# Performance work log

Hardware: AMD Instinct MI355X
Metric: run time of the kernel (lower is better)

The kernel has to match this reference:

```python
import jax, jax.numpy as jnp
import numpy as np

N, C, DK, DV = 8192, 128, 64, 64


def setup_inputs() -> dict:
    key = jax.random.key(0)
    ks = jax.random.split(key, 7)
    x = jax.random.normal(ks[0], (N, C), dtype=jnp.float32)
    # kaiming_normal for weights (std = sqrt(2/fan_in)), torch-default uniform bias
    std = float(np.sqrt(2.0 / C))
    bb = float(1.0 / np.sqrt(C))
    Wq = jax.random.normal(ks[1], (DK, C), dtype=jnp.float32) * std
    Wk = jax.random.normal(ks[2], (DK, C), dtype=jnp.float32) * std
    Wv = jax.random.normal(ks[3], (DV, C), dtype=jnp.float32) * std
    bq = jax.random.uniform(ks[4], (DK,), dtype=jnp.float32, minval=-bb, maxval=bb)
    bk = jax.random.uniform(ks[5], (DK,), dtype=jnp.float32, minval=-bb, maxval=bb)
    bv = jax.random.uniform(ks[6], (DV,), dtype=jnp.float32, minval=-bb, maxval=bb)
    return {"polyline_feature": x, "Wq": Wq, "bq": bq, "Wk": Wk, "bk": bk, "Wv": Wv, "bv": bv}


def reference(polyline_feature, Wq, bq, Wk, bk, Wv, bv):
    x = polyline_feature
    Q = jax.nn.relu(x @ Wq.T + bq)  # [N, DK]
    K = jax.nn.relu(x @ Wk.T + bk)  # [N, DK]
    V = jax.nn.relu(x @ Wv.T + bv)  # [N, DV]
    scores = (Q @ K.T) / jnp.sqrt(jnp.asarray(K.shape[1], Q.dtype))  # [N, N]
    attn = jax.nn.softmax(scores, axis=1)
    return attn @ V + Q  # residual on Q (non-standard)
```

## Files before the change

### kernel.cpp

```cpp
#include <hip/hip_runtime.h>


typedef __attribute__((ext_vector_type(8))) __bf16 bf16x8;
typedef __attribute__((ext_vector_type(4))) float f32x4;
typedef __attribute__((ext_vector_type(16))) float f32x16;

constexpr int N_ROWS = 8192;
constexpr int CDIM   = 128;
constexpr int DKV    = 64;
constexpr float SCALE_Q = 0.125f * 1.4426950408889634f;

__device__ __forceinline__ float fast_exp2(float x) {
    return __builtin_amdgcn_exp2f(x);
}

__device__ __forceinline__ unsigned short f2bf(float x) {
    union { float f; unsigned u; } v; v.f = x;
    unsigned r = v.u + 0x7fffu + ((v.u >> 16) & 1u);
    return (unsigned short)(r >> 16);
}

union Frag {
    unsigned u32[4];
    unsigned short u16[8];
    bf16x8 b;
    f32x4 f;
};

__global__ __launch_bounds__(128) void qkv_kernel(
    const float* __restrict__ x,
    const float* __restrict__ Wq, const float* __restrict__ bq,
    const float* __restrict__ Wk, const float* __restrict__ bk,
    const float* __restrict__ Wv, const float* __restrict__ bv,
    unsigned short* __restrict__ Qb, unsigned short* __restrict__ Kb,
    unsigned short* __restrict__ Vt, float* __restrict__ Qf)
{
    const int tid = threadIdx.x;
    const int w  = tid >> 6;
    const int l  = tid & 63;
    const int g  = l >> 4;
    const int lm = l & 15;
    const int n_base = blockIdx.x * 32 + w * 16;

    bf16x8 af[4];
    {
        const float* xrow = x + (size_t)(n_base + lm) * CDIM;
        #pragma unroll
        for (int s = 0; s < 4; ++s) {
            f32x4 lo = *(const f32x4*)(xrow + s * 32 + g * 8);
            f32x4 hi = *(const f32x4*)(xrow + s * 32 + g * 8 + 4);
            Frag fr;
            #pragma unroll
            for (int j = 0; j < 4; ++j) { fr.u16[j] = f2bf(lo[j]); fr.u16[4 + j] = f2bf(hi[j]); }
            af[s] = fr.b;
        }
    }

    const float* Ws[3] = {Wq, Wk, Wv};
    const float* Bs[3] = {bq, bk, bv};
    #pragma unroll
    for (int mat = 0; mat < 3; ++mat) {
        #pragma unroll
        for (int ct = 0; ct < 4; ++ct) {
            const int f = ct * 16 + lm;
            const float* wrow = Ws[mat] + (size_t)f * CDIM;
            f32x4 acc = {0.f, 0.f, 0.f, 0.f};
            #pragma unroll
            for (int s = 0; s < 4; ++s) {
                f32x4 lo = *(const f32x4*)(wrow + s * 32 + g * 8);
                f32x4 hi = *(const f32x4*)(wrow + s * 32 + g * 8 + 4);
                Frag fr;
                #pragma unroll
                for (int j = 0; j < 4; ++j) { fr.u16[j] = f2bf(lo[j]); fr.u16[4 + j] = f2bf(hi[j]); }
                acc = __builtin_amdgcn_mfma_f32_16x16x32_bf16(af[s], fr.b, acc, 0, 0, 0);
            }
            const float bias = Bs[mat][f];
            #pragma unroll
            for (int j = 0; j < 4; ++j) {
                const int n = n_base + g * 4 + j;
                const float v = fmaxf(acc[j] + bias, 0.f);
                if (mat == 0) {
                    Qf[(size_t)n * DKV + f] = v;
                    Qb[(size_t)n * DKV + f] = f2bf(v * SCALE_Q);
                } else if (mat == 1) {
                    Kb[(size_t)n * DKV + f] = f2bf(v);
                } else {
                    Vt[(size_t)f * N_ROWS + n] = f2bf(v);
                }
            }
        }
    }
}

__global__ __launch_bounds__(256, 4) void attn_kernel(
    const unsigned short* __restrict__ Qb, const unsigned short* __restrict__ Kb,
    const unsigned short* __restrict__ Vt,
    float* __restrict__ PartO, float* __restrict__ PartL,
    int kv_per_split)
{
    __shared__ __align__(16) unsigned short K_lds[2][64 * 64];
    __shared__ __align__(16) unsigned short V_lds[2][64 * 64];

    const int tid = threadIdx.x;
    const int w  = tid >> 6;
    const int l  = tid & 63;
    const int c  = l & 31;
    const int hB = l >> 5;
    const int qb = blockIdx.x;
    const int sp = blockIdx.y;
    const int q0 = qb * 128 + w * 32;
    const int kv0 = sp * kv_per_split;

    const int lrow = l >> 3;
    const int srcc = ((l & 7) ^ lrow) * 8;

#define ISSUE_LOADS(T, B) do { \
    const int kvt_ = kv0 + (T) * 64; \
    _Pragma("unroll") \
    for (int i = 0; i < 2; ++i) { \
        const int row_ = w * 16 + i * 8 + lrow; \
        __builtin_amdgcn_global_load_lds( \
            (const __attribute__((address_space(1))) unsigned int*)(Kb + (size_t)(kvt_ + row_) * DKV + srcc), \
            (__attribute__((address_space(3))) unsigned int*)&K_lds[B][(w * 16 + i * 8) * 64], 16, 0, 0); \
        __builtin_amdgcn_global_load_lds( \
            (const __attribute__((address_space(1))) unsigned int*)(Vt + (size_t)row_ * N_ROWS + kvt_ + srcc), \
            (__attribute__((address_space(3))) unsigned int*)&V_lds[B][(w * 16 + i * 8) * 64], 16, 0, 0); \
    } \
} while (0)

    bf16x8 qf0, qf1, qf2, qf3;
    {
        const unsigned short* qp = Qb + (size_t)(q0 + c) * DKV + hB * 8;
        qf0 = *(const bf16x8*)(qp);
        qf1 = *(const bf16x8*)(qp + 16);
        qf2 = *(const bf16x8*)(qp + 32);
        qf3 = *(const bf16x8*)(qp + 48);
    }

    f32x16 o0 = {}, o1 = {};
    float lsum = 0.f;

    const int nt = kv_per_split >> 6;
    ISSUE_LOADS(0, 0);
    if (nt > 1) ISSUE_LOADS(1, 1);
    __syncthreads();

    for (int t = 0; t < nt; ++t) {
        const char* Kl = (const char*)&K_lds[t & 1][0];
        const char* Vl = (const char*)&V_lds[t & 1][0];
        const int swz = (c & 7) << 4;

        f32x16 st0 = {}, st1 = {};
        #pragma unroll
        for (int ks = 0; ks < 4; ++ks) {
            const int cb = ks * 32 + hB * 16;
            bf16x8 a0 = *(const bf16x8*)(Kl + c * 128 + (cb ^ swz));
            bf16x8 a1 = *(const bf16x8*)(Kl + (32 + c) * 128 + (cb ^ swz));
            const bf16x8 qv = (ks == 0) ? qf0 : (ks == 1) ? qf1 : (ks == 2) ? qf2 : qf3;
            st0 = __builtin_amdgcn_mfma_f32_32x32x16_bf16(a0, qv, st0, 0, 0, 0);
            st1 = __builtin_amdgcn_mfma_f32_32x32x16_bf16(a1, qv, st1, 0, 0, 0);
        }

        unsigned pk[16];
        float ls = 0.f;
        #pragma unroll
        for (int p = 0; p < 8; ++p) {
            float a = fast_exp2(st0[2 * p]);
            float b = fast_exp2(st0[2 * p + 1]);
            ls += a + b;
            union { unsigned u; __bf16 h[2]; } uu;
            uu.h[0] = (__bf16)a; uu.h[1] = (__bf16)b;
            pk[p] = uu.u;
        }
        #pragma unroll
        for (int p = 0; p < 8; ++p) {
            float a = fast_exp2(st1[2 * p]);
            float b = fast_exp2(st1[2 * p + 1]);
            ls += a + b;
            union { unsigned u; __bf16 h[2]; } uu;
            uu.h[0] = (__bf16)a; uu.h[1] = (__bf16)b;
            pk[8 + p] = uu.u;
        }
        lsum += ls;

        #pragma unroll
        for (int ks = 0; ks < 4; ++ks) {
            const int base = (ks >> 1) * 8 + (ks & 1) * 4;
            const unsigned ownA  = hB ? pk[base + 2] : pk[base + 0];
            const unsigned ownB  = hB ? pk[base + 3] : pk[base + 1];
            const unsigned contA = hB ? pk[base + 0] : pk[base + 2];
            const unsigned contB = hB ? pk[base + 1] : pk[base + 3];
            const unsigned crossA = __shfl_xor(contA, 32);
            const unsigned crossB = __shfl_xor(contB, 32);
            Frag pf;
            pf.u32[0] = hB ? crossA : ownA;
            pf.u32[1] = hB ? crossB : ownB;
            pf.u32[2] = hB ? ownA : crossA;
            pf.u32[3] = hB ? ownB : crossB;
            const int cb = ks * 32 + hB * 16;
            bf16x8 a0 = *(const bf16x8*)(Vl + c * 128 + (cb ^ swz));
            bf16x8 a1 = *(const bf16x8*)(Vl + (32 + c) * 128 + (cb ^ swz));
            o0 = __builtin_amdgcn_mfma_f32_32x32x16_bf16(a0, pf.b, o0, 0, 0, 0);
            o1 = __builtin_amdgcn_mfma_f32_32x32x16_bf16(a1, pf.b, o1, 0, 0, 0);
        }

        __syncthreads();
        if (t + 2 < nt) ISSUE_LOADS(t + 2, t & 1);
    }
#undef ISSUE_LOADS

    lsum += __shfl_xor(lsum, 32);

    float* po = PartO + ((size_t)sp * N_ROWS + q0 + c) * 64;
    #pragma unroll
    for (int r = 0; r < 16; ++r) {
        const int dv = (r & 3) + 8 * (r >> 2) + 4 * hB;
        po[dv]      = o0[r];
        po[32 + dv] = o1[r];
    }
    if (hB == 0)
        PartL[(size_t)sp * N_ROWS + q0 + c] = lsum;
}

__global__ __launch_bounds__(256) void merge_kernel(
    const float* __restrict__ PartO, const float* __restrict__ PartL,
    const float* __restrict__ Qf, float* __restrict__ out, int split)
{
    const int gid = blockIdx.x * 256 + threadIdx.x;
    const int q = gid >> 6;
    const int d = gid & 63;

    float L = 0.f;
    float acc = 0.f;
    for (int s = 0; s < split; ++s) {
        L   += PartL[(size_t)s * N_ROWS + q];
        acc += PartO[((size_t)s * N_ROWS + q) * 64 + d];
    }
    out[(size_t)q * 64 + d] = acc / L + Qf[(size_t)q * 64 + d];
}

extern "C" void kernel_launch(void* const* d_in, const int* in_sizes, int n_in,
                              void* d_out, int out_size, void* d_ws, size_t ws_size,
                              hipStream_t stream)
{
    const float* x  = (const float*)d_in[0];
    const float* Wq = (const float*)d_in[1];
    const float* bq = (const float*)d_in[2];
    const float* Wk = (const float*)d_in[3];
    const float* bk = (const float*)d_in[4];
    const float* Wv = (const float*)d_in[5];
    const float* bv = (const float*)d_in[6];
    float* out = (float*)d_out;

    char* ws = (char*)d_ws;
    size_t off = 0;
    auto take = [&](size_t bytes) {
        char* p = ws + off;
        off += (bytes + 255) & ~(size_t)255;
        return p;
    };
    unsigned short* Qb = (unsigned short*)take((size_t)N_ROWS * DKV * 2);
    unsigned short* Kb = (unsigned short*)take((size_t)N_ROWS * DKV * 2);
    unsigned short* Vt = (unsigned short*)take((size_t)DKV * N_ROWS * 2);
    float*          Qf = (float*)take((size_t)N_ROWS * DKV * 4);

    int split = 16;
    const size_t per_split = (size_t)N_ROWS * 64 * 4 + (size_t)N_ROWS * 4 + 512;
    while (split > 1 && off + (size_t)split * per_split > ws_size) split >>= 1;

    float* PartO = (float*)take((size_t)split * N_ROWS * 64 * 4);
    float* PartL = (float*)take((size_t)split * N_ROWS * 4);

    qkv_kernel<<<dim3(N_ROWS / 32), dim3(128), 0, stream>>>(
        x, Wq, bq, Wk, bk, Wv, bv, Qb, Kb, Vt, Qf);
    attn_kernel<<<dim3(N_ROWS / 128, split), dim3(256), 0, stream>>>(
        Qb, Kb, Vt, PartO, PartL, N_ROWS / split);
    merge_kernel<<<dim3(N_ROWS * DKV / 256), dim3(256), 0, stream>>>(
        PartO, PartL, Qf, out, split);
}
```

Measured before the change: 50.12 us.

## Double query rows per wave, store bf16 partials, add MFMA priority hints

Each wave now handles 64 query rows instead of 32, so every K/V fragment loaded from LDS feeds twice as many MFMAs. The grid halves along the query axis and the occupancy hint drops from 4 to 2 blocks per CU to make room for the extra registers. Split partial outputs are written as bf16 to halve partial-buffer traffic, and the merge kernel reads packed pairs. s_setprio is raised around the MFMA groups. The cost is fewer concurrent waves and lower precision in the partial sums.

```diff
diff --git a/kernel.cpp b/kernel.cpp
--- a/kernel.cpp
+++ b/kernel.cpp
@@ -18,6 +18,10 @@
     union { float f; unsigned u; } v; v.f = x;
     unsigned r = v.u + 0x7fffu + ((v.u >> 16) & 1u);
     return (unsigned short)(r >> 16);
+}
+
+__device__ __forceinline__ float bf2f(unsigned short h) {
+    union { unsigned u; float f; } v; v.u = (unsigned)h << 16; return v.f;
 }
 
 union Frag {
@@ -92,10 +96,10 @@
     }
 }
 
-__global__ __launch_bounds__(256, 4) void attn_kernel(
+__global__ __launch_bounds__(256, 2) void attn_kernel(
     const unsigned short* __restrict__ Qb, const unsigned short* __restrict__ Kb,
     const unsigned short* __restrict__ Vt,
-    float* __restrict__ PartO, float* __restrict__ PartL,
+    unsigned short* __restrict__ PartOb, float* __restrict__ PartL,
     int kv_per_split)
 {
     __shared__ __align__(16) unsigned short K_lds[2][64 * 64];
@@ -108,7 +112,7 @@
     const int hB = l >> 5;
     const int qb = blockIdx.x;
     const int sp = blockIdx.y;
-    const int q0 = qb * 128 + w * 32;
+    const int q0 = qb * 256 + w * 64;
     const int kv0 = sp * kv_per_split;
 
     const int lrow = l >> 3;
@@ -128,17 +132,22 @@
     } \
 } while (0)
 
-    bf16x8 qf0, qf1, qf2, qf3;
+    bf16x8 qf0_0, qf0_1, qf0_2, qf0_3, qf1_0, qf1_1, qf1_2, qf1_3;
     {
-        const unsigned short* qp = Qb + (size_t)(q0 + c) * DKV + hB * 8;
-        qf0 = *(const bf16x8*)(qp);
-        qf1 = *(const bf16x8*)(qp + 16);
-        qf2 = *(const bf16x8*)(qp + 32);
-        qf3 = *(const bf16x8*)(qp + 48);
-    }
-
-    f32x16 o0 = {}, o1 = {};
-    float lsum = 0.f;
+        const unsigned short* qp0 = Qb + (size_t)(q0 + c) * DKV + hB * 8;
+        qf0_0 = *(const bf16x8*)(qp0);
+        qf0_1 = *(const bf16x8*)(qp0 + 16);
+        qf0_2 = *(const bf16x8*)(qp0 + 32);
+        qf0_3 = *(const bf16x8*)(qp0 + 48);
+        const unsigned short* qp1 = Qb + (size_t)(q0 + 32 + c) * DKV + hB * 8;
+        qf1_0 = *(const bf16x8*)(qp1);
+        qf1_1 = *(const bf16x8*)(qp1 + 16);
+        qf1_2 = *(const bf16x8*)(qp1 + 32);
+        qf1_3 = *(const bf16x8*)(qp1 + 48);
+    }
+
+    f32x16 o00 = {}, o01 = {}, o10 = {}, o11 = {};
+    float lsum0 = 0.f, lsum1 = 0.f;
 
     const int nt = kv_per_split >> 6;
     ISSUE_LOADS(0, 0);
@@ -150,58 +159,94 @@
         const char* Vl = (const char*)&V_lds[t & 1][0];
         const int swz = (c & 7) << 4;
 
-        f32x16 st0 = {}, st1 = {};
+        f32x16 s00 = {}, s01 = {}, s10 = {}, s11 = {};
+        __builtin_amdgcn_s_setprio(1);
         #pragma unroll
         for (int ks = 0; ks < 4; ++ks) {
             const int cb = ks * 32 + hB * 16;
             bf16x8 a0 = *(const bf16x8*)(Kl + c * 128 + (cb ^ swz));
             bf16x8 a1 = *(const bf16x8*)(Kl + (32 + c) * 128 + (cb ^ swz));
-            const bf16x8 qv = (ks == 0) ? qf0 : (ks == 1) ? qf1 : (ks == 2) ? qf2 : qf3;
-            st0 = __builtin_amdgcn_mfma_f32_32x32x16_bf16(a0, qv, st0, 0, 0, 0);
-            st1 = __builtin_amdgcn_mfma_f32_32x32x16_bf16(a1, qv, st1, 0, 0, 0);
-        }
-
-        unsigned pk[16];
-        float ls = 0.f;
+            const bf16x8 q0v = (ks == 0) ? qf0_0 : (ks == 1) ? qf0_1 : (ks == 2) ? qf0_2 : qf0_3;
+            const bf16x8 q1v = (ks == 0) ? qf1_0 : (ks == 1) ? qf1_1 : (ks == 2) ? qf1_2 : qf1_3;
+            s00 = __builtin_amdgcn_mfma_f32_32x32x16_bf16(a0, q0v, s00, 0, 0, 0);
+            s01 = __builtin_amdgcn_mfma_f32_32x32x16_bf16(a1, q0v, s01, 0, 0, 0);
+            s10 = __builtin_amdgcn_mfma_f32_32x32x16_bf16(a0, q1v, s10, 0, 0, 0);
+            s11 = __builtin_amdgcn_mfma_f32_32x32x16_bf16(a1, q1v, s11, 0, 0, 0);
+        }
+        __builtin_amdgcn_s_setprio(0);
+
+        unsigned pk0[16], pk1[16];
+        float ls0 = 0.f, ls1 = 0.f;
         #pragma unroll
         for (int p = 0; p < 8; ++p) {
-            float a = fast_exp2(st0[2 * p]);
-            float b = fast_exp2(st0[2 * p + 1]);
-            ls += a + b;
+            float a = fast_exp2(s00[2 * p]);
+            float b = fast_exp2(s00[2 * p + 1]);
+            ls0 += a + b;
             union { unsigned u; __bf16 h[2]; } uu;
             uu.h[0] = (__bf16)a; uu.h[1] = (__bf16)b;
-            pk[p] = uu.u;
+            pk0[p] = uu.u;
+            float a2 = fast_exp2(s01[2 * p]);
+            float b2 = fast_exp2(s01[2 * p + 1]);
+            ls0 += a2 + b2;
+            union { unsigned u; __bf16 h[2]; } uv;
+            uv.h[0] = (__bf16)a2; uv.h[1] = (__bf16)b2;
+            pk0[8 + p] = uv.u;
         }
         #pragma unroll
         for (int p = 0; p < 8; ++p) {
-            float a = fast_exp2(st1[2 * p]);
-            float b = fast_exp2(st1[2 * p + 1]);
-            ls += a + b;
+            float a = fast_exp2(s10[2 * p]);
+            float b = fast_exp2(s10[2 * p + 1]);
+            ls1 += a + b;
             union { unsigned u; __bf16 h[2]; } uu;
             uu.h[0] = (__bf16)a; uu.h[1] = (__bf16)b;
-            pk[8 + p] = uu.u;
-        }
-        lsum += ls;
+            pk1[p] = uu.u;
+            float a2 = fast_exp2(s11[2 * p]);
+            float b2 = fast_exp2(s11[2 * p + 1]);
+            ls1 += a2 + b2;
+            union { unsigned u; __bf16 h[2]; } uv;
+            uv.h[0] = (__bf16)a2; uv.h[1] = (__bf16)b2;
+            pk1[8 + p] = uv.u;
+        }
+        lsum0 += ls0;
+        lsum1 += ls1;
 
         #pragma unroll
         for (int ks = 0; ks < 4; ++ks) {
             const int base = (ks >> 1) * 8 + (ks & 1) * 4;
-            const unsigned ownA  = hB ? pk[base + 2] : pk[base + 0];
-            const unsigned ownB  = hB ? pk[base + 3] : pk[base + 1];
-            const unsigned contA = hB ? pk[base + 0] : pk[base + 2];
-            const unsigned contB = hB ? pk[base + 1] : pk[base + 3];
-            const unsigned crossA = __shfl_xor(contA, 32);
-            const unsigned crossB = __shfl_xor(contB, 32);
-            Frag pf;
-            pf.u32[0] = hB ? crossA : ownA;
-            pf.u32[1] = hB ? crossB : ownB;
-            pf.u32[2] = hB ? ownA : crossA;
-            pf.u32[3] = hB ? ownB : crossB;
+            Frag pf0, pf1;
+            {
+                const unsigned ownA  = hB ? pk0[base + 2] : pk0[base + 0];
+                const unsigned ownB  = hB ? pk0[base + 3] : pk0[base + 1];
+                const unsigned contA = hB ? pk0[base + 0] : pk0[base + 2];
+                const unsigned contB = hB ? pk0[base + 1] : pk0[base + 3];
+                const unsigned crossA = __shfl_xor(contA, 32);
+                const unsigned crossB = __shfl_xor(contB, 32);
+                pf0.u32[0] = hB ? crossA : ownA;
+                pf0.u32[1] = hB ? crossB : ownB;
+                pf0.u32[2] = hB ? ownA : crossA;
+                pf0.u32[3] = hB ? ownB : crossB;
+            }
+            {
+                const unsigned ownA  = hB ? pk1[base + 2] : pk1[base + 0];
+                const unsigned ownB  = hB ? pk1[base + 3] : pk1[base + 1];
+                const unsigned contA = hB ? pk1[base + 0] : pk1[base + 2];
+                const unsigned contB = hB ? pk1[base + 1] : pk1[base + 3];
+                const unsigned crossA = __shfl_xor(contA, 32);
+                const unsigned crossB = __shfl_xor(contB, 32);
+                pf1.u32[0] = hB ? crossA : ownA;
+                pf1.u32[1] = hB ? crossB : ownB;
+                pf1.u32[2] = hB ? ownA : crossA;
+                pf1.u32[3] = hB ? ownB : crossB;
+            }
             const int cb = ks * 32 + hB * 16;
-            bf16x8 a0 = *(const bf16x8*)(Vl + c * 128 + (cb ^ swz));
-            bf16x8 a1 = *(const bf16x8*)(Vl + (32 + c) * 128 + (cb ^ swz));
-            o0 = __builtin_amdgcn_mfma_f32_32x32x16_bf16(a0, pf.b, o0, 0, 0, 0);
-            o1 = __builtin_amdgcn_mfma_f32_32x32x16_bf16(a1, pf.b, o1, 0, 0, 0);
+            bf16x8 v0 = *(const bf16x8*)(Vl + c * 128 + (cb ^ swz));
+            bf16x8 v1 = *(const bf16x8*)(Vl + (32 + c) * 128 + (cb ^ swz));
+            __builtin_amdgcn_s_setprio(1);
+            o00 = __builtin_amdgcn_mfma_f32_32x32x16_bf16(v0, pf0.b, o00, 0, 0, 0);
+            o01 = __builtin_amdgcn_mfma_f32_32x32x16_bf16(v1, pf0.b, o01, 0, 0, 0);
+            o10 = __builtin_amdgcn_mfma_f32_32x32x16_bf16(v0, pf1.b, o10, 0, 0, 0);
+            o11 = __builtin_amdgcn_mfma_f32_32x32x16_bf16(v1, pf1.b, o11, 0, 0, 0);
+            __builtin_amdgcn_s_setprio(0);
         }
 
         __syncthreads();
@@ -209,34 +254,48 @@
     }
 #undef ISSUE_LOADS
 
-    lsum += __shfl_xor(lsum, 32);
-
-    float* po = PartO + ((size_t)sp * N_ROWS + q0 + c) * 64;
-    #pragma unroll
-    for (int r = 0; r < 16; ++r) {
-        const int dv = (r & 3) + 8 * (r >> 2) + 4 * hB;
-        po[dv]      = o0[r];
-        po[32 + dv] = o1[r];
-    }
-    if (hB == 0)
-        PartL[(size_t)sp * N_ROWS + q0 + c] = lsum;
+    lsum0 += __shfl_xor(lsum0, 32);
+    lsum1 += __shfl_xor(lsum1, 32);
+
+#define STORE_CG(OA, OB, CG) do { \
+    unsigned short* po = PartOb + ((size_t)sp * N_ROWS + q0 + 32 * (CG) + c) * 64; \
+    _Pragma("unroll") \
+    for (int rq = 0; rq < 4; ++rq) { \
+        union { unsigned u[2]; __bf16 h[4]; } pa, pb; \
+        _Pragma("unroll") \
+        for (int j = 0; j < 4; ++j) { pa.h[j] = (__bf16)OA[4 * rq + j]; pb.h[j] = (__bf16)OB[4 * rq + j]; } \
+        *(uint2*)(po + 8 * rq + 4 * hB)      = *(uint2*)pa.u; \
+        *(uint2*)(po + 32 + 8 * rq + 4 * hB) = *(uint2*)pb.u; \
+    } \
+} while (0)
+    STORE_CG(o00, o01, 0);
+    STORE_CG(o10, o11, 1);
+#undef STORE_CG
+    if (hB == 0) {
+        PartL[(size_t)sp * N_ROWS + q0 + c]      = lsum0;
+        PartL[(size_t)sp * N_ROWS + q0 + 32 + c] = lsum1;
+    }
 }
 
 __global__ __launch_bounds__(256) void merge_kernel(
-    const float* __restrict__ PartO, const float* __restrict__ PartL,
+    const unsigned short* __restrict__ PartOb, const float* __restrict__ PartL,
     const float* __restrict__ Qf, float* __restrict__ out, int split)
 {
     const int gid = blockIdx.x * 256 + threadIdx.x;
-    const int q = gid >> 6;
-    const int d = gid & 63;
-
-    float L = 0.f;
-    float acc = 0.f;
+    const int q  = gid >> 5;
+    const int dp = gid & 31;
+
+    float L = 0.f, a0 = 0.f, a1 = 0.f;
     for (int s = 0; s < split; ++s) {
-        L   += PartL[(size_t)s * N_ROWS + q];
-        acc += PartO[((size_t)s * N_ROWS + q) * 64 + d];
-    }
-    out[(size_t)q * 64 + d] = acc / L + Qf[(size_t)q * 64 + d];
+        L += PartL[(size_t)s * N_ROWS + q];
+        const unsigned v = *(const unsigned*)(PartOb + ((size_t)s * N_ROWS + q) * 64 + 2 * dp);
+        a0 += bf2f((unsigned short)(v & 0xffffu));
+        a1 += bf2f((unsigned short)(v >> 16));
+    }
+    const float invL = 1.f / L;
+    const int d0 = 2 * dp;
+    out[(size_t)q * 64 + d0]     = a0 * invL + Qf[(size_t)q * 64 + d0];
+    out[(size_t)q * 64 + d0 + 1] = a1 * invL + Qf[(size_t)q * 64 + d0 + 1];
 }
 
 extern "C" void kernel_launch(void* const* d_in, const int* in_sizes, int n_in,
@@ -265,16 +324,16 @@
     float*          Qf = (float*)take((size_t)N_ROWS * DKV * 4);
 
     int split = 16;
-    const size_t per_split = (size_t)N_ROWS * 64 * 4 + (size_t)N_ROWS * 4 + 512;
+    const size_t per_split = (size_t)N_ROWS * 64 * 2 + (size_t)N_ROWS * 4 + 512;
     while (split > 1 && off + (size_t)split * per_split > ws_size) split >>= 1;
 
-    float* PartO = (float*)take((size_t)split * N_ROWS * 64 * 4);
-    float* PartL = (float*)take((size_t)split * N_ROWS * 4);
+    unsigned short* PartOb = (unsigned short*)take((size_t)split * N_ROWS * 64 * 2);
+    float*          PartL  = (float*)take((size_t)split * N_ROWS * 4);
 
     qkv_kernel<<<dim3(N_ROWS / 32), dim3(128), 0, stream>>>(
         x, Wq, bq, Wk, bk, Wv, bv, Qb, Kb, Vt, Qf);
-    attn_kernel<<<dim3(N_ROWS / 128, split), dim3(256), 0, stream>>>(
-        Qb, Kb, Vt, PartO, PartL, N_ROWS / split);
-    merge_kernel<<<dim3(N_ROWS * DKV / 256), dim3(256), 0, stream>>>(
-        PartO, PartL, Qf, out, split);
-}
+    attn_kernel<<<dim3(N_ROWS / 256, split), dim3(256), 0, stream>>>(
+        Qb, Kb, Vt, PartOb, PartL, N_ROWS / split);
+    merge_kernel<<<dim3(N_ROWS * 32 / 256), dim3(256), 0, stream>>>(
+        PartOb, PartL, Qf, out, split);
+}
```

Measured after the change: 51.52 us. 2.8% more time.

## Widen attention blocks to 8 waves and store bf16 partial outputs

Applied to the files above, without the earlier changes.

The attention kernel now runs 512 threads per block covering 256 query rows, so each K/V tile loaded into LDS is shared by twice as many waves. Each wave loads one 8-row slice, and the LDS swizzle is adjusted to the new row mapping. Split partial outputs are written as packed bf16 instead of fp32, which halves the partial-result write and read traffic, and the merge kernel handles two columns per thread with a reciprocal. The cost is lower precision when summing partials and fewer blocks in the grid.

```diff
diff --git a/kernel.cpp b/kernel.cpp
--- a/kernel.cpp
+++ b/kernel.cpp
@@ -18,6 +18,10 @@
     union { float f; unsigned u; } v; v.f = x;
     unsigned r = v.u + 0x7fffu + ((v.u >> 16) & 1u);
     return (unsigned short)(r >> 16);
+}
+
+__device__ __forceinline__ float bf2f(unsigned short h) {
+    union { unsigned u; float f; } v; v.u = (unsigned)h << 16; return v.f;
 }
 
 union Frag {
@@ -92,10 +96,10 @@
     }
 }
 
-__global__ __launch_bounds__(256, 4) void attn_kernel(
+__global__ __launch_bounds__(512, 4) void attn_kernel(
     const unsigned short* __restrict__ Qb, const unsigned short* __restrict__ Kb,
     const unsigned short* __restrict__ Vt,
-    float* __restrict__ PartO, float* __restrict__ PartL,
+    unsigned short* __restrict__ PartOb, float* __restrict__ PartL,
     int kv_per_split)
 {
     __shared__ __align__(16) unsigned short K_lds[2][64 * 64];
@@ -108,24 +112,21 @@
     const int hB = l >> 5;
     const int qb = blockIdx.x;
     const int sp = blockIdx.y;
-    const int q0 = qb * 128 + w * 32;
+    const int q0 = qb * 256 + w * 32;
     const int kv0 = sp * kv_per_split;
 
-    const int lrow = l >> 3;
-    const int srcc = ((l & 7) ^ lrow) * 8;
+    const int r_ = w * 8 + (l >> 3);
+    const int perm_ = (r_ & 7) ^ (((r_ >> 3) & 3) << 1);
+    const int srcc = ((l & 7) ^ perm_) * 8;
 
 #define ISSUE_LOADS(T, B) do { \
     const int kvt_ = kv0 + (T) * 64; \
-    _Pragma("unroll") \
-    for (int i = 0; i < 2; ++i) { \
-        const int row_ = w * 16 + i * 8 + lrow; \
-        __builtin_amdgcn_global_load_lds( \
-            (const __attribute__((address_space(1))) unsigned int*)(Kb + (size_t)(kvt_ + row_) * DKV + srcc), \
-            (__attribute__((address_space(3))) unsigned int*)&K_lds[B][(w * 16 + i * 8) * 64], 16, 0, 0); \
-        __builtin_amdgcn_global_load_lds( \
-            (const __attribute__((address_space(1))) unsigned int*)(Vt + (size_t)row_ * N_ROWS + kvt_ + srcc), \
-            (__attribute__((address_space(3))) unsigned int*)&V_lds[B][(w * 16 + i * 8) * 64], 16, 0, 0); \
-    } \
+    __builtin_amdgcn_global_load_lds( \
+        (const __attribute__((address_space(1))) unsigned int*)(Kb + (size_t)(kvt_ + r_) * DKV + srcc), \
+        (__attribute__((address_space(3))) unsigned int*)&K_lds[B][w * 8 * 64], 16, 0, 0); \
+    __builtin_amdgcn_global_load_lds( \
+        (const __attribute__((address_space(1))) unsigned int*)(Vt + (size_t)r_ * N_ROWS + kvt_ + srcc), \
+        (__attribute__((address_space(3))) unsigned int*)&V_lds[B][w * 8 * 64], 16, 0, 0); \
 } while (0)
 
     bf16x8 qf0, qf1, qf2, qf3;
@@ -145,10 +146,11 @@
     if (nt > 1) ISSUE_LOADS(1, 1);
     __syncthreads();
 
+    const int swz = ((c & 7) ^ (((c >> 3) & 3) << 1)) << 4;
+
     for (int t = 0; t < nt; ++t) {
         const char* Kl = (const char*)&K_lds[t & 1][0];
         const char* Vl = (const char*)&V_lds[t & 1][0];
-        const int swz = (c & 7) << 4;
 
         f32x16 st0 = {}, st1 = {};
         #pragma unroll
@@ -198,10 +200,10 @@
             pf.u32[2] = hB ? ownA : crossA;
             pf.u32[3] = hB ? ownB : crossB;
             const int cb = ks * 32 + hB * 16;
-            bf16x8 a0 = *(const bf16x8*)(Vl + c * 128 + (cb ^ swz));
-            bf16x8 a1 = *(const bf16x8*)(Vl + (32 + c) * 128 + (cb ^ swz));
-            o0 = __builtin_amdgcn_mfma_f32_32x32x16_bf16(a0, pf.b, o0, 0, 0, 0);
-            o1 = __builtin_amdgcn_mfma_f32_32x32x16_bf16(a1, pf.b, o1, 0, 0, 0);
+            bf16x8 v0 = *(const bf16x8*)(Vl + c * 128 + (cb ^ swz));
+            bf16x8 v1 = *(const bf16x8*)(Vl + (32 + c) * 128 + (cb ^ swz));
+            o0 = __builtin_amdgcn_mfma_f32_32x32x16_bf16(v0, pf.b, o0, 0, 0, 0);
+            o1 = __builtin_amdgcn_mfma_f32_32x32x16_bf16(v1, pf.b, o1, 0, 0, 0);
         }
 
         __syncthreads();
@@ -211,32 +213,40 @@
 
     lsum += __shfl_xor(lsum, 32);
 
-    float* po = PartO + ((size_t)sp * N_ROWS + q0 + c) * 64;
-    #pragma unroll
-    for (int r = 0; r < 16; ++r) {
-        const int dv = (r & 3) + 8 * (r >> 2) + 4 * hB;
-        po[dv]      = o0[r];
-        po[32 + dv] = o1[r];
+    {
+        unsigned short* po = PartOb + ((size_t)sp * N_ROWS + q0 + c) * 64;
+        #pragma unroll
+        for (int rq = 0; rq < 4; ++rq) {
+            union { unsigned u[2]; __bf16 h[4]; } pa, pb;
+            #pragma unroll
+            for (int j = 0; j < 4; ++j) { pa.h[j] = (__bf16)o0[4 * rq + j]; pb.h[j] = (__bf16)o1[4 * rq + j]; }
+            *(uint2*)(po + 8 * rq + 4 * hB)      = *(uint2*)pa.u;
+            *(uint2*)(po + 32 + 8 * rq + 4 * hB) = *(uint2*)pb.u;
+        }
     }
     if (hB == 0)
         PartL[(size_t)sp * N_ROWS + q0 + c] = lsum;
 }
 
 __global__ __launch_bounds__(256) void merge_kernel(
-    const float* __restrict__ PartO, const float* __restrict__ PartL,
+    const unsigned short* __restrict__ PartOb, const float* __restrict__ PartL,
     const float* __restrict__ Qf, float* __restrict__ out, int split)
 {
     const int gid = blockIdx.x * 256 + threadIdx.x;
-    const int q = gid >> 6;
-    const int d = gid & 63;
-
-    float L = 0.f;
-    float acc = 0.f;
+    const int q  = gid >> 5;
+    const int dp = gid & 31;
+
+    float L = 0.f, a0 = 0.f, a1 = 0.f;
     for (int s = 0; s < split; ++s) {
-        L   += PartL[(size_t)s * N_ROWS + q];
-        acc += PartO[((size_t)s * N_ROWS + q) * 64 + d];
-    }
-    out[(size_t)q * 64 + d] = acc / L + Qf[(size_t)q * 64 + d];
+        L += PartL[(size_t)s * N_ROWS + q];
+        const unsigned v = *(const unsigned*)(PartOb + ((size_t)s * N_ROWS + q) * 64 + 2 * dp);
+        a0 += bf2f((unsigned short)(v & 0xffffu));
+        a1 += bf2f((unsigned short)(v >> 16));
+    }
+    const float invL = 1.f / L;
+    const int d0 = 2 * dp;
+    out[(size_t)q * 64 + d0]     = a0 * invL + Qf[(size_t)q * 64 + d0];
+    out[(size_t)q * 64 + d0 + 1] = a1 * invL + Qf[(size_t)q * 64 + d0 + 1];
 }
 
 extern "C" void kernel_launch(void* const* d_in, const int* in_sizes, int n_in,
@@ -265,16 +275,16 @@
     float*          Qf = (float*)take((size_t)N_ROWS * DKV * 4);
 
     int split = 16;
-    const size_t per_split = (size_t)N_ROWS * 64 * 4 + (size_t)N_ROWS * 4 + 512;
+    const size_t per_split = (size_t)N_ROWS * 64 * 2 + (size_t)N_ROWS * 4 + 512;
     while (split > 1 && off + (size_t)split * per_split > ws_size) split >>= 1;
 
-    float* PartO = (float*)take((size_t)split * N_ROWS * 64 * 4);
-    float* PartL = (float*)take((size_t)split * N_ROWS * 4);
+    unsigned short* PartOb = (unsigned short*)take((size_t)split * N_ROWS * 64 * 2);
+    float*          PartL  = (float*)take((size_t)split * N_ROWS * 4);
 
     qkv_kernel<<<dim3(N_ROWS / 32), dim3(128), 0, stream>>>(
         x, Wq, bq, Wk, bk, Wv, bv, Qb, Kb, Vt, Qf);
-    attn_kernel<<<dim3(N_ROWS / 128, split), dim3(256), 0, stream>>>(
-        Qb, Kb, Vt, PartO, PartL, N_ROWS / split);
-    merge_kernel<<<dim3(N_ROWS * DKV / 256), dim3(256), 0, stream>>>(
-        PartO, PartL, Qf, out, split);
-}
+    attn_kernel<<<dim3(N_ROWS / 256, split), dim3(512), 0, stream>>>(
+        Qb, Kb, Vt, PartOb, PartL, N_ROWS / split);
+    merge_kernel<<<dim3(N_ROWS * 32 / 256), dim3(256), 0, stream>>>(
+        PartOb, PartL, Qf, out, split);
+}
```

After: 49.39 us. Within noise of the previous version (-1.5%).
